# Optimization experiments

Hardware: AMD Instinct MI355X
Metric: run time of the kernel (lower is better)

Reference implementation:

```python
import jax, jax.numpy as jnp
import numpy as np

N = 100_000   # nodes
E = 1_200_000 # edges
D = 64        # in_dim
H = 64        # hidden_dim
B = 1000      # graphs in batch
C = 10        # num_classes
TOPO = 64     # topo_dim
BN_EPS = 1e-5


def setup_inputs() -> dict:
    key = jax.random.key(0)
    ks = jax.random.split(key, 24)
    x = jax.random.normal(ks[0], (N, D), dtype=jnp.float32)
    edge_index = jax.random.randint(ks[1], (2, E), 0, N, dtype=jnp.int32)
    # sorted graph ids; force last id = B-1 so batch.max()+1 == B (matches torch path)
    batch = jnp.sort(jax.random.randint(ks[2], (N,), 0, B, dtype=jnp.int32)).at[-1].set(B - 1)
    topo = jax.random.normal(ks[3], (B, TOPO), dtype=jnp.float32)
    s = 0.05
    return {
        "x": x, "edge_index": edge_index, "batch": batch, "topo": topo,
        # conv1 MLP: Linear(D,H) -> BN(H) -> ReLU -> Linear(H,H) -> ReLU
        "W1a": jax.random.normal(ks[4], (D, H)) * s, "b1a": jax.random.normal(ks[5], (H,)) * s,
        "g1": 1.0 + jax.random.normal(ks[6], (H,)) * s, "be1": jax.random.normal(ks[7], (H,)) * s,
        "m1": jax.random.normal(ks[8], (H,)) * s, "v1": 0.5 + jax.random.uniform(ks[9], (H,)),
        "W1b": jax.random.normal(ks[10], (H, H)) * s, "b1b": jax.random.normal(ks[11], (H,)) * s,
        # conv2 MLP: Linear(H,H) -> BN(H) -> ReLU
        "W2": jax.random.normal(ks[12], (H, H)) * s, "b2": jax.random.normal(ks[13], (H,)) * s,
        "g2": 1.0 + jax.random.normal(ks[14], (H,)) * s, "be2": jax.random.normal(ks[15], (H,)) * s,
        "m2": jax.random.normal(ks[16], (H,)) * s, "v2": 0.5 + jax.random.uniform(ks[17], (H,)),
        # topo_net: Linear(TOPO,H) -> ReLU
        "Wt": jax.random.normal(ks[18], (TOPO, H)) * s, "bt": jax.random.normal(ks[19], (H,)) * s,
        # classifier: Linear(2H, C)
        "Wc": jax.random.normal(ks[20], (2 * H, C)) * s, "bc": jax.random.normal(ks[21], (C,)) * s,
    }


def _bn_eval(v, g, b, m, var):
    # BatchNorm1d in eval mode: affine with running stats
    return g * (v - m) * jax.lax.rsqrt(var + BN_EPS) + b


def _gin_agg(h, src, dst):
    # GINConv (eps=0): (1+eps)*x_i + sum_{j->i} x_j ; scatter-add over dst
    return h + jax.ops.segment_sum(h[src], dst, num_segments=N)


def reference(x, edge_index, batch, topo,
              W1a, b1a, g1, be1, m1, v1, W1b, b1b,
              W2, b2, g2, be2, m2, v2, Wt, bt, Wc, bc):
    src, dst = edge_index[0], edge_index[1]
    # conv1: MLP(agg(x)) = Lin -> BN -> ReLU -> Lin -> ReLU; outer relu from forward
    h = _gin_agg(x, src, dst)                              # [N, D]
    h = jax.nn.relu(_bn_eval(h @ W1a + b1a, g1, be1, m1, v1))
    h = jax.nn.relu(h @ W1b + b1b)                         # [N, H]
    h = jax.nn.relu(h)                                     # F.relu(conv1(...))
    # dropout(p=0.5) is identity in eval mode
    # conv2: Lin -> BN -> ReLU, then outer relu
    h = _gin_agg(h, src, dst)                              # [N, H]
    h = jax.nn.relu(_bn_eval(h @ W2 + b2, g2, be2, m2, v2))
    h = jax.nn.relu(h)
    # global_add_pool: sum nodes per graph
    x_struct = jax.ops.segment_sum(h, batch, num_segments=B)   # [B, H]
    # topo already [B, TOPO] => all reshape/pad branches are no-ops
    x_topo = jax.nn.relu(topo @ Wt + bt)                   # [B, H]
    combined = jnp.concatenate([x_struct, x_topo], axis=1) # [B, 2H]
    return combined @ Wc + bc                              # [B, C]
```

## Files before the change

kernel.cpp:

```cpp
#include <hip/hip_runtime.h>

#define N_NODES 100000
#define N_EDGES 1200000
#define DIM     64
#define BGRAPHS 1000
#define NCLASS  10
#define BN_EPS  1e-5f

#define NBUCK   256
#define NPB     391
#define MAGIC   10984572u
#define CHUNK   8192
#define NBLK_P  147
#define CAP     8192
#define NB_G    1563

typedef __attribute__((ext_vector_type(8))) short   bfx8;
typedef __attribute__((ext_vector_type(4))) float   f32x4;
typedef __attribute__((ext_vector_type(8))) unsigned short u16x8;

__device__ __forceinline__ unsigned short f2bf(float f) {
    unsigned u = __builtin_bit_cast(unsigned, f);
    unsigned r = (u + 0x7FFFu + ((u >> 16) & 1u)) >> 16;
    return (unsigned short)r;
}
__device__ __forceinline__ float bf2f(unsigned short h) {
    unsigned u = ((unsigned)h) << 16;
    return __builtin_bit_cast(float, u);
}

__device__ __forceinline__ bfx8 load_wfrag(const float* __restrict__ W, int kt, int q, int col) {
    bfx8 f;
    #pragma unroll
    for (int j = 0; j < 8; ++j)
        f[j] = (short)f2bf(W[(kt * 32 + q * 8 + j) * 64 + col]);
    return f;
}

__global__ __launch_bounds__(256) void prep_kernel(
    const float* __restrict__ x, const int* __restrict__ ei,
    int* __restrict__ gpart,
    const float* __restrict__ W1a, unsigned short* __restrict__ y0,
    float* __restrict__ xs,
    const float* __restrict__ W1b, const float* __restrict__ W2,
    unsigned short* __restrict__ w1bp, unsigned short* __restrict__ w2p,
    const float* __restrict__ b1a, const float* __restrict__ g1,
    const float* __restrict__ be1, const float* __restrict__ m1,
    const float* __restrict__ v1,
    const float* __restrict__ b2,  const float* __restrict__ g2,
    const float* __restrict__ be2, const float* __restrict__ m2,
    const float* __restrict__ v2,
    float* __restrict__ AB, int* __restrict__ cursor) {
    __shared__ int cnt[NBUCK];
    __shared__ unsigned short outt[4][16 * 64];
    int t = threadIdx.x;
    if (blockIdx.x < NBLK_P) {
        int blk = blockIdx.x;
        cnt[t] = 0;
        __syncthreads();
        int e0 = blk * CHUNK;
        for (int i = t; i < CHUNK; i += 256) {
            int e = e0 + i;
            if (e >= N_EDGES) break;
            unsigned d = (unsigned)ei[N_EDGES + e];
            atomicAdd(&cnt[__umulhi(d, MAGIC)], 1);
        }
        __syncthreads();
        gpart[blk * NBUCK + t] = cnt[t];
    } else if (blockIdx.x < NBLK_P + NB_G) {
        int g = blockIdx.x - NBLK_P;
        if (g < (BGRAPHS * DIM) / 256) xs[g * 256 + t] = 0.f;
        int w = t >> 6, lane = t & 63;
        int m = lane & 15, q = lane >> 4;
        int row0 = g * 64 + w * 16;

        bfx8 wa[4][2];
        #pragma unroll
        for (int nt = 0; nt < 4; ++nt)
            #pragma unroll
            for (int kt = 0; kt < 2; ++kt)
                wa[nt][kt] = load_wfrag(W1a, kt, q, nt * 16 + m);

        int rowA = row0 + m;
        if (rowA > N_NODES - 1) rowA = N_NODES - 1;
        const float* xp = x + (long long)rowA * 64;
        bfx8 a0, a1;
        #pragma unroll
        for (int j = 0; j < 8; ++j) {
            a0[j] = (short)f2bf(xp[q * 8 + j]);
            a1[j] = (short)f2bf(xp[32 + q * 8 + j]);
        }
        f32x4 acc[4];
        #pragma unroll
        for (int nt = 0; nt < 4; ++nt) {
            acc[nt] = (f32x4){0.f, 0.f, 0.f, 0.f};
            acc[nt] = __builtin_amdgcn_mfma_f32_16x16x32_bf16(a0, wa[nt][0], acc[nt], 0, 0, 0);
            acc[nt] = __builtin_amdgcn_mfma_f32_16x16x32_bf16(a1, wa[nt][1], acc[nt], 0, 0, 0);
        }
        #pragma unroll
        for (int nt = 0; nt < 4; ++nt)
            #pragma unroll
            for (int r = 0; r < 4; ++r)
                outt[w][(q * 4 + r) * 64 + nt * 16 + m] = f2bf(acc[nt][r]);
        __syncthreads();
        #pragma unroll
        for (int i = lane; i < 128; i += 64) {
            int rr = i >> 3, cc = i & 7;
            int rg = row0 + rr;
            if (rg < N_NODES)
                ((float4*)y0)[(long long)rg * 8 + cc] = *(const float4*)&outt[w][rr * 64 + cc * 8];
        }
    } else {
        cursor[t] = 0;
        const float* Ws[2] = {W1b, W2};
        unsigned short* Wp[2] = {w1bp, w2p};
        #pragma unroll
        for (int wsel = 0; wsel < 2; ++wsel) {
            const float* W = Ws[wsel];
            #pragma unroll
            for (int r = 0; r < 2; ++r) {
                int e = r * 256 + t;
                int kt = e >> 8, q = (e >> 6) & 3, col = e & 63;
                u16x8 o;
                #pragma unroll
                for (int j = 0; j < 8; ++j)
                    o[j] = f2bf(W[(kt * 32 + q * 8 + j) * 64 + col]);
                ((u16x8*)Wp[wsel])[e] = o;
            }
        }
        if (t < 64) {
            float s1 = g1[t] * rsqrtf(v1[t] + BN_EPS);
            AB[t]       = s1;
            AB[64 + t]  = b1a[t] * s1 + (be1[t] - m1[t] * s1);
            float s2 = g2[t] * rsqrtf(v2[t] + BN_EPS);
            AB[128 + t] = s2;
            AB[192 + t] = b2[t] * s2 + (be2[t] - m2[t] * s2);
        }
    }
}

__global__ __launch_bounds__(256) void part_kernel(const int* __restrict__ ei,
                                                   const int* __restrict__ gpart,
                                                   int* __restrict__ cursor,
                                                   int* __restrict__ base,
                                                   int* __restrict__ srcbuf,
                                                   unsigned short* __restrict__ dstlbuf) {
    __shared__ int tmp[256];
    __shared__ int cur[NBUCK];
    int t = threadIdx.x, blk = blockIdx.x;
    int s = 0;
    for (int b = 0; b < NBLK_P; ++b) s += gpart[b * NBUCK + t];
    tmp[t] = s;
    __syncthreads();
    for (int off = 1; off < 256; off <<= 1) {
        int a = (t >= off) ? tmp[t - off] : 0;
        __syncthreads();
        tmp[t] += a;
        __syncthreads();
    }
    int excl = tmp[t] - s;
    base[t] = excl;
    if (blk == 0 && t == 255) base[256] = N_EDGES;
    int resv = atomicAdd(&cursor[t], gpart[blk * NBUCK + t]);
    cur[t] = excl + resv;
    __syncthreads();
    int e0 = blk * CHUNK;
    for (int i = t; i < CHUNK; i += 256) {
        int e = e0 + i;
        if (e >= N_EDGES) break;
        unsigned d = (unsigned)ei[N_EDGES + e];
        int sv = ei[e];
        int b = __umulhi(d, MAGIC);
        int pos = atomicAdd(&cur[b], 1);
        srcbuf[pos] = sv;
        dstlbuf[pos] = (unsigned short)(d - b * NPB);
    }
}

__global__ __launch_bounds__(256) void refine_kernel(const int* __restrict__ srcbuf,
                                                     const unsigned short* __restrict__ dstlbuf,
                                                     const int* __restrict__ base,
                                                     int* __restrict__ csr_src,
                                                     int* __restrict__ rowptr) {
    __shared__ int cnt[NPB + 1];
    __shared__ int cur[NPB + 1];
    __shared__ int tmp[256];
    __shared__ int outb[CAP];
    int t = threadIdx.x, b = blockIdx.x;
    int beg = base[b];
    int end = base[b + 1];

    for (int i = t; i < NPB + 1; i += 256) cnt[i] = 0;
    __syncthreads();
    for (int i = beg + t; i < end; i += 256)
        atomicAdd(&cnt[dstlbuf[i]], 1);
    __syncthreads();

    int i0 = 2 * t, i1 = 2 * t + 1;
    int v0 = (i0 < NPB) ? cnt[i0] : 0;
    int v1 = (i1 < NPB) ? cnt[i1] : 0;
    int s = v0 + v1;
    tmp[t] = s;
    __syncthreads();
    for (int off = 1; off < 256; off <<= 1) {
        int a = (t >= off) ? tmp[t - off] : 0;
        __syncthreads();
        tmp[t] += a;
        __syncthreads();
    }
    int excl = tmp[t] - s;
    if (i0 < NPB) cur[i0] = excl;
    if (i1 < NPB) cur[i1] = excl + v0;
    {
        int g0 = b * NPB + i0;
        if (i0 < NPB && g0 < N_NODES) rowptr[g0] = beg + excl;
        int g1 = b * NPB + i1;
        if (i1 < NPB && g1 < N_NODES) rowptr[g1] = beg + excl + v0;
    }
    if (b == NBUCK - 1 && t == 0) rowptr[N_NODES] = N_EDGES;
    __syncthreads();

    for (int i = beg + t; i < end; i += 256) {
        int dl = dstlbuf[i];
        int pos = atomicAdd(&cur[dl], 1);
        if (pos < CAP) outb[pos] = srcbuf[i];
    }
    __syncthreads();

    int nb = end - beg; if (nb > CAP) nb = CAP;
    for (int i = t; i < nb; i += 256) csr_src[beg + i] = outb[i];
}

__global__ __launch_bounds__(256) void gather_mlp1_kernel(
    const unsigned short* __restrict__ feat,
    const int* __restrict__ rowptr, const int* __restrict__ csr_src,
    const float* __restrict__ AB,
    const unsigned short* __restrict__ w1bp, const float* __restrict__ b1b,
    const unsigned short* __restrict__ w2p,
    unsigned short* __restrict__ y2) {
    __shared__ unsigned short h1t[32 * 72];
    __shared__ unsigned short h2t[32 * 72];
    __shared__ unsigned short outt[32 * 64];

    int t = threadIdx.x;
    int nl = t >> 3, q8 = t & 7;
    int node = blockIdx.x * 32 + nl;
    const u16x8* f8 = (const u16x8*)feat;
    {
        u16x8 sv = f8[(long long)node * 8 + q8];
        float acc[8];
        #pragma unroll
        for (int j = 0; j < 8; ++j) acc[j] = bf2f(sv[j]);
        int beg = rowptr[node], end = rowptr[node + 1];
        int k = beg;
        int sn = (k < end) ? csr_src[k] : 0;
        while (k < end) {
            int sc = sn;
            ++k;
            if (k < end) sn = csr_src[k];
            u16x8 v = f8[(long long)sc * 8 + q8];
            #pragma unroll
            for (int j = 0; j < 8; ++j) acc[j] += bf2f(v[j]);
        }
        #pragma unroll
        for (int j = 0; j < 8; ++j) {
            int c = q8 * 8 + j;
            h1t[nl * 72 + c] = f2bf(fmaxf(acc[j] * AB[c] + AB[64 + c], 0.f));
        }
    }
    __syncthreads();

    int w = t >> 6, lane = t & 63;
    int m = lane & 15, q = lane >> 4;
    int rt = w >> 1;
    int c0 = (w & 1) * 2;

    const bfx8* wbp = (const bfx8*)w1bp;
    const bfx8* wcp = (const bfx8*)w2p;

    {
        const bfx8* hp = (const bfx8*)&h1t[(rt * 16 + m) * 72];
        bfx8 a0 = hp[q];
        bfx8 a1 = hp[4 + q];
        #pragma unroll
        for (int ci = 0; ci < 2; ++ci) {
            int ct = c0 + ci;
            bfx8 w0 = wbp[(0 * 4 + q) * 64 + ct * 16 + m];
            bfx8 w1 = wbp[(1 * 4 + q) * 64 + ct * 16 + m];
            f32x4 acc = (f32x4){0.f, 0.f, 0.f, 0.f};
            acc = __builtin_amdgcn_mfma_f32_16x16x32_bf16(a0, w0, acc, 0, 0, 0);
            acc = __builtin_amdgcn_mfma_f32_16x16x32_bf16(a1, w1, acc, 0, 0, 0);
            float bb = b1b[ct * 16 + m];
            #pragma unroll
            for (int r = 0; r < 4; ++r)
                h2t[(rt * 16 + q * 4 + r) * 72 + ct * 16 + m] = f2bf(fmaxf(acc[r] + bb, 0.f));
        }
    }
    __syncthreads();

    {
        const bfx8* hp = (const bfx8*)&h2t[(rt * 16 + m) * 72];
        bfx8 a0 = hp[q];
        bfx8 a1 = hp[4 + q];
        #pragma unroll
        for (int ci = 0; ci < 2; ++ci) {
            int ct = c0 + ci;
            bfx8 w0 = wcp[(0 * 4 + q) * 64 + ct * 16 + m];
            bfx8 w1 = wcp[(1 * 4 + q) * 64 + ct * 16 + m];
            f32x4 acc = (f32x4){0.f, 0.f, 0.f, 0.f};
            acc = __builtin_amdgcn_mfma_f32_16x16x32_bf16(a0, w0, acc, 0, 0, 0);
            acc = __builtin_amdgcn_mfma_f32_16x16x32_bf16(a1, w1, acc, 0, 0, 0);
            #pragma unroll
            for (int r = 0; r < 4; ++r)
                outt[(rt * 16 + q * 4 + r) * 64 + ct * 16 + m] = f2bf(acc[r]);
        }
    }
    __syncthreads();

    int rr = t >> 3, cc = t & 7;
    ((float4*)y2)[((long long)blockIdx.x * 32 + rr) * 8 + cc] =
        *(const float4*)&outt[rr * 64 + cc * 8];
}

__global__ __launch_bounds__(256) void gather_pool_kernel(
    const unsigned short* __restrict__ feat,
    const int* __restrict__ rowptr, const int* __restrict__ csr_src,
    const float* __restrict__ AB, const int* __restrict__ batch,
    float* __restrict__ xs) {
    __shared__ float h4[32 * 65];
    __shared__ int bts[32];
    int t = threadIdx.x;
    int nl = t >> 3;
    int q = t & 7;
    int node = blockIdx.x * 32 + nl;
    if (t < 32) bts[t] = batch[blockIdx.x * 32 + t];
    const u16x8* f8 = (const u16x8*)feat;
    u16x8 sv = f8[(long long)node * 8 + q];
    float acc[8];
    #pragma unroll
    for (int j = 0; j < 8; ++j) acc[j] = bf2f(sv[j]);
    int beg = rowptr[node], end = rowptr[node + 1];
    int k = beg;
    int sn = (k < end) ? csr_src[k] : 0;
    while (k < end) {
        int sc = sn;
        ++k;
        if (k < end) sn = csr_src[k];
        u16x8 v = f8[(long long)sc * 8 + q];
        #pragma unroll
        for (int j = 0; j < 8; ++j) acc[j] += bf2f(v[j]);
    }
    #pragma unroll
    for (int j = 0; j < 8; ++j) {
        int c = q * 8 + j;
        h4[nl * 65 + c] = fmaxf(acc[j] * AB[128 + c] + AB[192 + c], 0.f);
    }
    __syncthreads();

    int col = t & 63;
    int r0 = (t >> 6) * 8;
    int cb = bts[r0];
    float cur = 0.f;
    #pragma unroll
    for (int r = 0; r < 8; ++r) {
        int b = bts[r0 + r];
        if (b != cb) {
            unsafeAtomicAdd(&xs[cb * 64 + col], cur);
            cb = b;
            cur = 0.f;
        }
        cur += h4[(r0 + r) * 65 + col];
    }
    unsafeAtomicAdd(&xs[cb * 64 + col], cur);
}

__global__ __launch_bounds__(64) void head_kernel(
    const float* __restrict__ xs, const float* __restrict__ topo,
    const float* __restrict__ Wt, const float* __restrict__ bt,
    const float* __restrict__ Wc, const float* __restrict__ bc,
    float* __restrict__ out) {
    __shared__ float trow[64];
    __shared__ float comb[128];
    int b = blockIdx.x;
    int h = threadIdx.x;
    trow[h] = topo[b * 64 + h];
    __syncthreads();
    float acc = bt[h];
    #pragma unroll
    for (int k = 0; k < 64; ++k) acc += trow[k] * Wt[k * 64 + h];
    comb[h] = xs[b * 64 + h];
    comb[64 + h] = fmaxf(acc, 0.f);
    __syncthreads();
    if (h < NCLASS) {
        float o = bc[h];
        #pragma unroll
        for (int k = 0; k < 128; ++k) o += comb[k] * Wc[k * NCLASS + h];
        out[b * NCLASS + h] = o;
    }
}

extern "C" void kernel_launch(void* const* d_in, const int* in_sizes, int n_in,
                              void* d_out, int out_size, void* d_ws, size_t ws_size,
                              hipStream_t stream) {
    const float* x     = (const float*)d_in[0];
    const int*   ei    = (const int*)d_in[1];
    const int*   batch = (const int*)d_in[2];
    const float* topo  = (const float*)d_in[3];
    const float* W1a   = (const float*)d_in[4];
    const float* b1a   = (const float*)d_in[5];
    const float* g1    = (const float*)d_in[6];
    const float* be1   = (const float*)d_in[7];
    const float* m1    = (const float*)d_in[8];
    const float* v1    = (const float*)d_in[9];
    const float* W1b   = (const float*)d_in[10];
    const float* b1b   = (const float*)d_in[11];
    const float* W2    = (const float*)d_in[12];
    const float* b2    = (const float*)d_in[13];
    const float* g2    = (const float*)d_in[14];
    const float* be2   = (const float*)d_in[15];
    const float* m2    = (const float*)d_in[16];
    const float* v2    = (const float*)d_in[17];
    const float* Wt    = (const float*)d_in[18];
    const float* bt    = (const float*)d_in[19];
    const float* Wc    = (const float*)d_in[20];
    const float* bc    = (const float*)d_in[21];
    float* out = (float*)d_out;

    char* p = (char*)d_ws;
    unsigned short* y0   = (unsigned short*)p; p += (size_t)N_NODES * DIM * 2;
    unsigned short* y2b  = (unsigned short*)p; p += (size_t)N_NODES * DIM * 2;
    float* xs      = (float*)p; p += (size_t)BGRAPHS * DIM * 4;
    int*   rowptr  = (int*)p;   p += (size_t)(N_NODES + 16) * 4;
    int*   gpart   = (int*)p;   p += (size_t)NBLK_P * NBUCK * 4;
    int*   base    = (int*)p;   p += 1040;
    int*   cursor  = (int*)p;   p += 1024;
    unsigned short* w1bp = (unsigned short*)p; p += 512 * 16;
    unsigned short* w2p  = (unsigned short*)p; p += 512 * 16;
    float* AB      = (float*)p; p += 256 * 4;
    int*   srcbuf  = (int*)p;   p += (size_t)N_EDGES * 4;
    unsigned short* dstlbuf = (unsigned short*)p; p += (size_t)N_EDGES * 2;
    int*   csr_src = (int*)p;

    prep_kernel<<<NBLK_P + NB_G + 1, 256, 0, stream>>>(
        x, ei, gpart, W1a, y0, xs, W1b, W2, w1bp, w2p,
        b1a, g1, be1, m1, v1, b2, g2, be2, m2, v2, AB, cursor);
    part_kernel<<<NBLK_P, 256, 0, stream>>>(ei, gpart, cursor, base, srcbuf, dstlbuf);
    refine_kernel<<<NBUCK, 256, 0, stream>>>(srcbuf, dstlbuf, base, csr_src, rowptr);
    gather_mlp1_kernel<<<N_NODES / 32, 256, 0, stream>>>(
        y0, rowptr, csr_src, AB, w1bp, b1b, w2p, y2b);
    gather_pool_kernel<<<N_NODES / 32, 256, 0, stream>>>(y2b, rowptr, csr_src, AB, batch, xs);
    head_kernel<<<BGRAPHS, 64, 0, stream>>>(xs, topo, Wt, bt, Wc, bc, out);
}
```

Before: 228.9 us.

## Replace global bucket prefix scan with fixed-capacity bucket slots and per-row end pointers

```diff
diff --git a/kernel.cpp b/kernel.cpp
--- a/kernel.cpp
+++ b/kernel.cpp
@@ -12,7 +12,7 @@
 #define MAGIC   10984572u
 #define CHUNK   8192
 #define NBLK_P  147
-#define CAP     8192
+#define BCAP    8192
 #define NB_G    1563
 
 typedef __attribute__((ext_vector_type(8))) short   bfx8;
@@ -38,8 +38,7 @@
 }
 
 __global__ __launch_bounds__(256) void prep_kernel(
-    const float* __restrict__ x, const int* __restrict__ ei,
-    int* __restrict__ gpart,
+    const float* __restrict__ x,
     const float* __restrict__ W1a, unsigned short* __restrict__ y0,
     float* __restrict__ xs,
     const float* __restrict__ W1b, const float* __restrict__ W2,
@@ -51,24 +50,10 @@
     const float* __restrict__ be2, const float* __restrict__ m2,
     const float* __restrict__ v2,
     float* __restrict__ AB, int* __restrict__ cursor) {
-    __shared__ int cnt[NBUCK];
     __shared__ unsigned short outt[4][16 * 64];
     int t = threadIdx.x;
-    if (blockIdx.x < NBLK_P) {
-        int blk = blockIdx.x;
-        cnt[t] = 0;
-        __syncthreads();
-        int e0 = blk * CHUNK;
-        for (int i = t; i < CHUNK; i += 256) {
-            int e = e0 + i;
-            if (e >= N_EDGES) break;
-            unsigned d = (unsigned)ei[N_EDGES + e];
-            atomicAdd(&cnt[__umulhi(d, MAGIC)], 1);
-        }
-        __syncthreads();
-        gpart[blk * NBUCK + t] = cnt[t];
-    } else if (blockIdx.x < NBLK_P + NB_G) {
-        int g = blockIdx.x - NBLK_P;
+    if (blockIdx.x < NB_G) {
+        int g = blockIdx.x;
         if (g < (BGRAPHS * DIM) / 256) xs[g * 256 + t] = 0.f;
         int w = t >> 6, lane = t & 63;
         int m = lane & 15, q = lane >> 4;
@@ -111,7 +96,7 @@
                 ((float4*)y0)[(long long)rg * 8 + cc] = *(const float4*)&outt[w][rr * 64 + cc * 8];
         }
     } else {
-        cursor[t] = 0;
+        cursor[t] = t * BCAP;
         const float* Ws[2] = {W1b, W2};
         unsigned short* Wp[2] = {w1bp, w2p};
         #pragma unroll
@@ -140,31 +125,24 @@
 }
 
 __global__ __launch_bounds__(256) void part_kernel(const int* __restrict__ ei,
-                                                   const int* __restrict__ gpart,
                                                    int* __restrict__ cursor,
-                                                   int* __restrict__ base,
                                                    int* __restrict__ srcbuf,
                                                    unsigned short* __restrict__ dstlbuf) {
-    __shared__ int tmp[256];
+    __shared__ int cnt[NBUCK];
     __shared__ int cur[NBUCK];
     int t = threadIdx.x, blk = blockIdx.x;
-    int s = 0;
-    for (int b = 0; b < NBLK_P; ++b) s += gpart[b * NBUCK + t];
-    tmp[t] = s;
-    __syncthreads();
-    for (int off = 1; off < 256; off <<= 1) {
-        int a = (t >= off) ? tmp[t - off] : 0;
-        __syncthreads();
-        tmp[t] += a;
-        __syncthreads();
-    }
-    int excl = tmp[t] - s;
-    base[t] = excl;
-    if (blk == 0 && t == 255) base[256] = N_EDGES;
-    int resv = atomicAdd(&cursor[t], gpart[blk * NBUCK + t]);
-    cur[t] = excl + resv;
+    cnt[t] = 0;
     __syncthreads();
     int e0 = blk * CHUNK;
+    for (int i = t; i < CHUNK; i += 256) {
+        int e = e0 + i;
+        if (e >= N_EDGES) break;
+        unsigned d = (unsigned)ei[N_EDGES + e];
+        atomicAdd(&cnt[__umulhi(d, MAGIC)], 1);
+    }
+    __syncthreads();
+    cur[t] = atomicAdd(&cursor[t], cnt[t]);
+    __syncthreads();
     for (int i = t; i < CHUNK; i += 256) {
         int e = e0 + i;
         if (e >= N_EDGES) break;
@@ -179,16 +157,17 @@
 
 __global__ __launch_bounds__(256) void refine_kernel(const int* __restrict__ srcbuf,
                                                      const unsigned short* __restrict__ dstlbuf,
-                                                     const int* __restrict__ base,
+                                                     const int* __restrict__ cursor,
                                                      int* __restrict__ csr_src,
-                                                     int* __restrict__ rowptr) {
+                                                     int* __restrict__ rowptr,
+                                                     int* __restrict__ rowend) {
     __shared__ int cnt[NPB + 1];
     __shared__ int cur[NPB + 1];
     __shared__ int tmp[256];
-    __shared__ int outb[CAP];
+    __shared__ int outb[BCAP];
     int t = threadIdx.x, b = blockIdx.x;
-    int beg = base[b];
-    int end = base[b + 1];
+    int beg = b * BCAP;
+    int end = cursor[b];
 
     for (int i = t; i < NPB + 1; i += 256) cnt[i] = 0;
     __syncthreads();
@@ -213,27 +192,33 @@
     if (i1 < NPB) cur[i1] = excl + v0;
     {
         int g0 = b * NPB + i0;
-        if (i0 < NPB && g0 < N_NODES) rowptr[g0] = beg + excl;
+        if (i0 < NPB && g0 < N_NODES) {
+            rowptr[g0] = beg + excl;
+            rowend[g0] = beg + excl + v0;
+        }
         int g1 = b * NPB + i1;
-        if (i1 < NPB && g1 < N_NODES) rowptr[g1] = beg + excl + v0;
-    }
-    if (b == NBUCK - 1 && t == 0) rowptr[N_NODES] = N_EDGES;
+        if (i1 < NPB && g1 < N_NODES) {
+            rowptr[g1] = beg + excl + v0;
+            rowend[g1] = beg + excl + v0 + v1;
+        }
+    }
     __syncthreads();
 
     for (int i = beg + t; i < end; i += 256) {
         int dl = dstlbuf[i];
         int pos = atomicAdd(&cur[dl], 1);
-        if (pos < CAP) outb[pos] = srcbuf[i];
-    }
-    __syncthreads();
-
-    int nb = end - beg; if (nb > CAP) nb = CAP;
+        if (pos < BCAP) outb[pos] = srcbuf[i];
+    }
+    __syncthreads();
+
+    int nb = end - beg; if (nb > BCAP) nb = BCAP;
     for (int i = t; i < nb; i += 256) csr_src[beg + i] = outb[i];
 }
 
 __global__ __launch_bounds__(256) void gather_mlp1_kernel(
     const unsigned short* __restrict__ feat,
-    const int* __restrict__ rowptr, const int* __restrict__ csr_src,
+    const int* __restrict__ rowptr, const int* __restrict__ rowend,
+    const int* __restrict__ csr_src,
     const float* __restrict__ AB,
     const unsigned short* __restrict__ w1bp, const float* __restrict__ b1b,
     const unsigned short* __restrict__ w2p,
@@ -251,7 +236,7 @@
         float acc[8];
         #pragma unroll
         for (int j = 0; j < 8; ++j) acc[j] = bf2f(sv[j]);
-        int beg = rowptr[node], end = rowptr[node + 1];
+        int beg = rowptr[node], end = rowend[node];
         int k = beg;
         int sn = (k < end) ? csr_src[k] : 0;
         while (k < end) {
@@ -324,7 +309,8 @@
 
 __global__ __launch_bounds__(256) void gather_pool_kernel(
     const unsigned short* __restrict__ feat,
-    const int* __restrict__ rowptr, const int* __restrict__ csr_src,
+    const int* __restrict__ rowptr, const int* __restrict__ rowend,
+    const int* __restrict__ csr_src,
     const float* __restrict__ AB, const int* __restrict__ batch,
     float* __restrict__ xs) {
     __shared__ float h4[32 * 65];
@@ -339,7 +325,7 @@
     float acc[8];
     #pragma unroll
     for (int j = 0; j < 8; ++j) acc[j] = bf2f(sv[j]);
-    int beg = rowptr[node], end = rowptr[node + 1];
+    int beg = rowptr[node], end = rowend[node];
     int k = beg;
     int sn = (k < end) ? csr_src[k] : 0;
     while (k < end) {
@@ -431,23 +417,23 @@
     unsigned short* y2b  = (unsigned short*)p; p += (size_t)N_NODES * DIM * 2;
     float* xs      = (float*)p; p += (size_t)BGRAPHS * DIM * 4;
     int*   rowptr  = (int*)p;   p += (size_t)(N_NODES + 16) * 4;
-    int*   gpart   = (int*)p;   p += (size_t)NBLK_P * NBUCK * 4;
-    int*   base    = (int*)p;   p += 1040;
+    int*   rowend  = (int*)p;   p += (size_t)(N_NODES + 16) * 4;
     int*   cursor  = (int*)p;   p += 1024;
     unsigned short* w1bp = (unsigned short*)p; p += 512 * 16;
     unsigned short* w2p  = (unsigned short*)p; p += 512 * 16;
     float* AB      = (float*)p; p += 256 * 4;
-    int*   srcbuf  = (int*)p;   p += (size_t)N_EDGES * 4;
-    unsigned short* dstlbuf = (unsigned short*)p; p += (size_t)N_EDGES * 2;
+    int*   srcbuf  = (int*)p;   p += (size_t)NBUCK * BCAP * 4;
+    unsigned short* dstlbuf = (unsigned short*)p; p += (size_t)NBUCK * BCAP * 2;
     int*   csr_src = (int*)p;
 
-    prep_kernel<<<NBLK_P + NB_G + 1, 256, 0, stream>>>(
-        x, ei, gpart, W1a, y0, xs, W1b, W2, w1bp, w2p,
+    prep_kernel<<<NB_G + 1, 256, 0, stream>>>(
+        x, W1a, y0, xs, W1b, W2, w1bp, w2p,
         b1a, g1, be1, m1, v1, b2, g2, be2, m2, v2, AB, cursor);
-    part_kernel<<<NBLK_P, 256, 0, stream>>>(ei, gpart, cursor, base, srcbuf, dstlbuf);
-    refine_kernel<<<NBUCK, 256, 0, stream>>>(srcbuf, dstlbuf, base, csr_src, rowptr);
+    part_kernel<<<NBLK_P, 256, 0, stream>>>(ei, cursor, srcbuf, dstlbuf);
+    refine_kernel<<<NBUCK, 256, 0, stream>>>(srcbuf, dstlbuf, cursor, csr_src, rowptr, rowend);
     gather_mlp1_kernel<<<N_NODES / 32, 256, 0, stream>>>(
-        y0, rowptr, csr_src, AB, w1bp, b1b, w2p, y2b);
-    gather_pool_kernel<<<N_NODES / 32, 256, 0, stream>>>(y2b, rowptr, csr_src, AB, batch, xs);
+        y0, rowptr, rowend, csr_src, AB, w1bp, b1b, w2p, y2b);
+    gather_pool_kernel<<<N_NODES / 32, 256, 0, stream>>>(
+        y2b, rowptr, rowend, csr_src, AB, batch, xs);
     head_kernel<<<BGRAPHS, 64, 0, stream>>>(xs, topo, Wt, bt, Wc, bc, out);
 }
```

Measured after the change: 225.5 us. No clear change (-1.5%).
